# Kernel tuning notes

Measured on AMD Instinct MI355X. Metric: run time of the kernel, lower is better.

Reference implementation:

```python
import jax, jax.numpy as jnp
import numpy as np

# Gemma-2B style config
B, S, HID = 2, 2048, 2048
H, KH, D = 8, 1, 256          # query heads, kv heads, head_dim
THETA = 10000.0


def setup_inputs() -> dict:
    key = jax.random.key(0)
    ks = jax.random.split(key, 6)
    s = 0.02  # init scale for weights
    return {
        "hidden_states": jax.random.normal(ks[0], (B, S, HID), dtype=jnp.float32),
        "attention_mask": jnp.zeros((B, S), dtype=jnp.float32),  # additive mask over kv axis
        "position_ids": jnp.broadcast_to(jnp.arange(S, dtype=jnp.int32), (B, S)),
        "Wq": jax.random.normal(ks[1], (H * D, HID), dtype=jnp.float32) * s,
        "bq": jnp.zeros((H * D,), dtype=jnp.float32),
        "Wk": jax.random.normal(ks[2], (KH * D, HID), dtype=jnp.float32) * s,
        "bk": jnp.zeros((KH * D,), dtype=jnp.float32),
        "Wv": jax.random.normal(ks[3], (KH * D, HID), dtype=jnp.float32) * s,
        "bv": jnp.zeros((KH * D,), dtype=jnp.float32),
        "Wo": jax.random.normal(ks[4], (HID, H * D), dtype=jnp.float32) * s,
        "bo": jnp.zeros((HID,), dtype=jnp.float32),
    }


def _rope(x, position_ids):
    # x: [b, s, h, d]; rotate-half RoPE per head, computed in fp32 as in the module.
    half = D // 2
    inv_freq = 1.0 / (THETA ** (jnp.arange(0, D, 2, dtype=jnp.float32) / D))  # [d/2]
    freqs = position_ids.astype(jnp.float32)[:, :, None] * inv_freq            # [b, s, d/2]
    cos = jnp.cos(freqs)[:, :, None, :]  # [b, s, 1, d/2]
    sin = jnp.sin(freqs)[:, :, None, :]
    x1, x2 = x[..., :half], x[..., half:]
    return jnp.concatenate([cos * x1 - sin * x2, sin * x1 + cos * x2], axis=-1).astype(x.dtype)


def reference(hidden_states, attention_mask, position_ids, Wq, bq, Wk, bk, Wv, bv, Wo, bo):
    b, s, _ = hidden_states.shape
    q = (hidden_states @ Wq.T + bq).reshape(b, s, H, D)
    k = (hidden_states @ Wk.T + bk).reshape(b, s, KH, D)
    v = (hidden_states @ Wv.T + bv).reshape(b, s, KH, D)
    q = _rope(q, position_ids)
    k = _rope(k, position_ids)
    # GQA: broadcast the KV heads across query-head groups
    groups = H // KH
    k = jnp.repeat(k, groups, axis=2)  # [b, s, H, D]
    v = jnp.repeat(v, groups, axis=2)
    scores = jnp.einsum('bnhd,bmhd->bhnm', q, k) * (D ** -0.5)  # [b, H, s, s]
    scores = scores + attention_mask[:, None, None, :]
    attn = jax.nn.softmax(scores, axis=-1)  # dropout p=0.0 -> identity
    out = jnp.einsum('bhnm,bmhd->bnhd', attn, v).reshape(b, s, H * D)
    out = out @ Wo.T + bo
    return (out, attn)
```

## Files before the change

kernel.cpp:

```cpp
#include <hip/hip_runtime.h>

#define B_ 2
#define S_ 2048
#define HID_ 2048
#define H_ 8
#define D_ 256

typedef unsigned short u16;
typedef __attribute__((ext_vector_type(8))) short bf16x8;
typedef __attribute__((ext_vector_type(4))) float f32x4;

__device__ __forceinline__ u16 f2b(float x) {
    unsigned u = __float_as_uint(x);
    unsigned rb = (u >> 16) & 1u;
    u += 0x7fffu + rb;
    return (u16)(u >> 16);
}

__global__ __launch_bounds__(256) void cvt_bf16(const float* __restrict__ in,
                                                u16* __restrict__ out, int n) {
    int i = (blockIdx.x * 256 + threadIdx.x) * 4;
    if (i >= n) return;
    float4 f = *(const float4*)(in + i);
    union { u16 u[4]; uint2 v; } pk;
    pk.u[0] = f2b(f.x); pk.u[1] = f2b(f.y); pk.u[2] = f2b(f.z); pk.u[3] = f2b(f.w);
    *(uint2*)(out + i) = pk.v;
}

__global__ __launch_bounds__(256) void rope_kernel(const float* __restrict__ x,
                                                   const int* __restrict__ pos_ids,
                                                   u16* __restrict__ out, int nHeads) {
    int idx = blockIdx.x * 256 + threadIdx.x;
    int d   = idx & 127;
    int tmp = idx >> 7;
    int h   = tmp % nHeads;
    int n   = tmp / nHeads;
    int pos = pos_ids[n];
    float ang = (float)pos * expf(-(float)d * (9.210340371976184f / 128.0f));
    float s, c;
    sincosf(ang, &s, &c);
    size_t base = ((size_t)n * nHeads + h) * D_;
    float x1 = x[base + d], x2 = x[base + d + 128];
    out[base + d]       = f2b(c * x1 - s * x2);
    out[base + d + 128] = f2b(s * x1 + c * x2);
}

__global__ __launch_bounds__(256) void transpose_v(const float* __restrict__ v,
                                                   u16* __restrict__ vT) {
    __shared__ float t[32][33];
    int b = blockIdx.z;
    int s0 = blockIdx.x * 32, d0 = blockIdx.y * 32;
    int tx = threadIdx.x, ty = threadIdx.y;
#pragma unroll
    for (int i = 0; i < 4; ++i)
        t[ty + i * 8][tx] = v[(size_t)b * S_ * D_ + (size_t)(s0 + ty + i * 8) * D_ + d0 + tx];
    __syncthreads();
#pragma unroll
    for (int i = 0; i < 4; ++i)
        vT[(size_t)b * D_ * S_ + (size_t)(d0 + ty + i * 8) * S_ + s0 + tx] = f2b(t[tx][ty + i * 8]);
}

__global__ __launch_bounds__(256) void softmax_rows(float* __restrict__ attn,
                                                    const float* __restrict__ mask) {
    int row = blockIdx.x;
    int b = row >> 14;
    float* p = attn + (size_t)row * S_;
    const float* mb = mask + (size_t)b * S_;
    int t = threadIdx.x;
    const float sc = 0.0625f;

    float4 v0 = *(float4*)(p + t * 4);
    float4 v1 = *(float4*)(p + 1024 + t * 4);
    float4 m0 = *(const float4*)(mb + t * 4);
    float4 m1 = *(const float4*)(mb + 1024 + t * 4);
    float x[8] = { v0.x * sc + m0.x, v0.y * sc + m0.y, v0.z * sc + m0.z, v0.w * sc + m0.w,
                   v1.x * sc + m1.x, v1.y * sc + m1.y, v1.z * sc + m1.z, v1.w * sc + m1.w };

    float mx = x[0];
#pragma unroll
    for (int j = 1; j < 8; ++j) mx = fmaxf(mx, x[j]);
#pragma unroll
    for (int o = 32; o > 0; o >>= 1) mx = fmaxf(mx, __shfl_down(mx, o));
    __shared__ float redm[4], reds[4];
    int lane = t & 63, w = t >> 6;
    if (lane == 0) redm[w] = mx;
    __syncthreads();
    mx = fmaxf(fmaxf(redm[0], redm[1]), fmaxf(redm[2], redm[3]));

    float e[8], s = 0.f;
#pragma unroll
    for (int j = 0; j < 8; ++j) { e[j] = expf(x[j] - mx); s += e[j]; }
#pragma unroll
    for (int o = 32; o > 0; o >>= 1) s += __shfl_down(s, o);
    if (lane == 0) reds[w] = s;
    __syncthreads();
    s = reds[0] + reds[1] + reds[2] + reds[3];
    float inv = 1.f / s;

    float4 o0 = { e[0] * inv, e[1] * inv, e[2] * inv, e[3] * inv };
    float4 o1 = { e[4] * inv, e[5] * inv, e[6] * inv, e[7] * inv };
    *(float4*)(p + t * 4) = o0;
    *(float4*)(p + 1024 + t * 4) = o1;
}

#define TILE_M 128
#define TILE_N 128
#define TILE_K 32
#define LDSK 40

template <bool A_IS_F32, bool C_IS_BF16>
__global__ __launch_bounds__(256, 2) void gemm_bt(
    const void* __restrict__ Ap, const u16* __restrict__ Bp, void* __restrict__ Cp,
    const float* __restrict__ bias, int M, int N, int K, int lda, int ldb, int ldc,
    long sAb, long sAh, long sBb, long sBh, long sCb, long sCh, int numH) {
    __shared__ __align__(16) u16 As[TILE_M * LDSK];
    __shared__ __align__(16) u16 Bs[TILE_N * LDSK];

    int z = blockIdx.z;
    int bb = z / numH, hh = z % numH;
    const u16* A16 = nullptr;
    const float* Af = nullptr;
    if constexpr (A_IS_F32) Af = (const float*)Ap + (long)bb * sAb + (long)hh * sAh;
    else                    A16 = (const u16*)Ap + (long)bb * sAb + (long)hh * sAh;
    const u16* Bb = Bp + (long)bb * sBb + (long)hh * sBh;
    char* Cb = (char*)Cp;
    long cOff = (long)bb * sCb + (long)hh * sCh;

    const int m0 = blockIdx.y * TILE_M;
    const int n0 = blockIdx.x * TILE_N;
    const int tid = threadIdx.x;
    const int lane = tid & 63, wave = tid >> 6;
    const int l15 = lane & 15, quad = lane >> 4;
    const int waveM = wave >> 1, waveN = wave & 1;

    f32x4 acc[4][4];
#pragma unroll
    for (int mt = 0; mt < 4; ++mt)
#pragma unroll
        for (int nt = 0; nt < 4; ++nt)
#pragma unroll
            for (int r = 0; r < 4; ++r) acc[mt][nt][r] = 0.f;

    for (int k0 = 0; k0 < K; k0 += TILE_K) {
#pragma unroll
        for (int i = 0; i < 2; ++i) {
            int c = tid + i * 256;
            int row = c >> 2, col = (c & 3) * 8;
            if constexpr (A_IS_F32) {
                const float* src = Af + (size_t)(m0 + row) * lda + k0 + col;
                float4 f0 = *(const float4*)src;
                float4 f1 = *(const float4*)(src + 4);
                union { u16 u[8]; uint4 v; } pk;
                pk.u[0] = f2b(f0.x); pk.u[1] = f2b(f0.y); pk.u[2] = f2b(f0.z); pk.u[3] = f2b(f0.w);
                pk.u[4] = f2b(f1.x); pk.u[5] = f2b(f1.y); pk.u[6] = f2b(f1.z); pk.u[7] = f2b(f1.w);
                *(uint4*)&As[row * LDSK + col] = pk.v;
            } else {
                *(uint4*)&As[row * LDSK + col] =
                    *(const uint4*)(A16 + (size_t)(m0 + row) * lda + k0 + col);
            }
            *(uint4*)&Bs[row * LDSK + col] =
                *(const uint4*)(Bb + (size_t)(n0 + row) * ldb + k0 + col);
        }
        __syncthreads();

        bf16x8 av[4], bv[4];
#pragma unroll
        for (int t = 0; t < 4; ++t) {
            av[t] = *(bf16x8*)&As[(waveM * 64 + t * 16 + l15) * LDSK + quad * 8];
            bv[t] = *(bf16x8*)&Bs[(waveN * 64 + t * 16 + l15) * LDSK + quad * 8];
        }
#pragma unroll
        for (int mt = 0; mt < 4; ++mt)
#pragma unroll
            for (int nt = 0; nt < 4; ++nt)
                acc[mt][nt] = __builtin_amdgcn_mfma_f32_16x16x32_bf16(av[mt], bv[nt],
                                                                      acc[mt][nt], 0, 0, 0);
        __syncthreads();
    }

#pragma unroll
    for (int mt = 0; mt < 4; ++mt) {
        int row = m0 + waveM * 64 + mt * 16 + quad * 4;
#pragma unroll
        for (int nt = 0; nt < 4; ++nt) {
            int col = n0 + waveN * 64 + nt * 16 + l15;
            float bia = bias ? bias[col] : 0.f;
#pragma unroll
            for (int r = 0; r < 4; ++r) {
                float val = acc[mt][nt][r] + bia;
                if constexpr (C_IS_BF16)
                    ((u16*)Cb)[cOff + (size_t)(row + r) * ldc + col] = f2b(val);
                else
                    ((float*)Cb)[cOff + (size_t)(row + r) * ldc + col] = val;
            }
        }
    }
}

extern "C" void kernel_launch(void* const* d_in, const int* in_sizes, int n_in,
                              void* d_out, int out_size, void* d_ws, size_t ws_size,
                              hipStream_t stream) {
    const float* hs   = (const float*)d_in[0];
    const float* mask = (const float*)d_in[1];
    const int*   pos  = (const int*)d_in[2];
    const float* Wq = (const float*)d_in[3];
    const float* bq = (const float*)d_in[4];
    const float* Wk = (const float*)d_in[5];
    const float* bk = (const float*)d_in[6];
    const float* Wv = (const float*)d_in[7];
    const float* bv = (const float*)d_in[8];
    const float* Wo = (const float*)d_in[9];
    const float* bo = (const float*)d_in[10];

    float* out  = (float*)d_out;
    float* attn = (float*)d_out + (size_t)B_ * S_ * HID_;

    char* ws = (char*)d_ws;
    u16* hs_b   = (u16*)ws;                       ws += (size_t)B_ * S_ * HID_ * 2;
    u16* Wq_b   = (u16*)ws;                       ws += (size_t)H_ * D_ * HID_ * 2;
    u16* Wk_b   = (u16*)ws;                       ws += (size_t)D_ * HID_ * 2;
    u16* Wv_b   = (u16*)ws;                       ws += (size_t)D_ * HID_ * 2;
    u16* Wo_b   = (u16*)ws;                       ws += (size_t)HID_ * H_ * D_ * 2;
    float* q_f  = (float*)ws;                     ws += (size_t)B_ * S_ * H_ * D_ * 4;
    float* k_f  = (float*)ws;                     ws += (size_t)B_ * S_ * D_ * 4;
    float* v_f  = (float*)ws;                     ws += (size_t)B_ * S_ * D_ * 4;
    u16* q_b    = (u16*)ws;                       ws += (size_t)B_ * S_ * H_ * D_ * 2;
    u16* k_b    = (u16*)ws;                       ws += (size_t)B_ * S_ * D_ * 2;
    u16* vT_b   = (u16*)ws;                       ws += (size_t)B_ * D_ * S_ * 2;
    u16* ctx_b  = hs_b;

    cvt_bf16<<<dim3((B_ * S_ * HID_) / 1024), 256, 0, stream>>>(hs, hs_b, B_ * S_ * HID_);
    cvt_bf16<<<dim3((H_ * D_ * HID_) / 1024), 256, 0, stream>>>(Wq, Wq_b, H_ * D_ * HID_);
    cvt_bf16<<<dim3((D_ * HID_) / 1024), 256, 0, stream>>>(Wk, Wk_b, D_ * HID_);
    cvt_bf16<<<dim3((D_ * HID_) / 1024), 256, 0, stream>>>(Wv, Wv_b, D_ * HID_);
    cvt_bf16<<<dim3((HID_ * H_ * D_) / 1024), 256, 0, stream>>>(Wo, Wo_b, HID_ * H_ * D_);

    gemm_bt<false, false><<<dim3((H_ * D_) / TILE_N, (B_ * S_) / TILE_M, 1), 256, 0, stream>>>(
        hs_b, Wq_b, q_f, bq, B_ * S_, H_ * D_, HID_, HID_, HID_, H_ * D_,
        0, 0, 0, 0, 0, 0, 1);
    gemm_bt<false, false><<<dim3(D_ / TILE_N, (B_ * S_) / TILE_M, 1), 256, 0, stream>>>(
        hs_b, Wk_b, k_f, bk, B_ * S_, D_, HID_, HID_, HID_, D_,
        0, 0, 0, 0, 0, 0, 1);
    gemm_bt<false, false><<<dim3(D_ / TILE_N, (B_ * S_) / TILE_M, 1), 256, 0, stream>>>(
        hs_b, Wv_b, v_f, bv, B_ * S_, D_, HID_, HID_, HID_, D_,
        0, 0, 0, 0, 0, 0, 1);

    rope_kernel<<<dim3((B_ * S_ * H_ * 128) / 256), 256, 0, stream>>>(q_f, pos, q_b, H_);
    rope_kernel<<<dim3((B_ * S_ * 1 * 128) / 256), 256, 0, stream>>>(k_f, pos, k_b, 1);
    transpose_v<<<dim3(S_ / 32, D_ / 32, B_), dim3(32, 8), 0, stream>>>(v_f, vT_b);

    gemm_bt<false, false><<<dim3(S_ / TILE_N, S_ / TILE_M, B_ * H_), 256, 0, stream>>>(
        q_b, k_b, attn, nullptr, S_, S_, D_, H_ * D_, D_, S_,
        (long)S_ * H_ * D_, D_,
        (long)S_ * D_, 0,
        (long)H_ * S_ * S_, (long)S_ * S_,
        H_);

    softmax_rows<<<dim3(B_ * H_ * S_), 256, 0, stream>>>(attn, mask);

    gemm_bt<true, true><<<dim3(D_ / TILE_N, S_ / TILE_M, B_ * H_), 256, 0, stream>>>(
        attn, vT_b, ctx_b, nullptr, S_, D_, S_, S_, S_, H_ * D_,
        (long)H_ * S_ * S_, (long)S_ * S_,
        (long)D_ * S_, 0,
        (long)S_ * H_ * D_, D_,
        H_);

    gemm_bt<false, false><<<dim3(HID_ / TILE_N, (B_ * S_) / TILE_M, 1), 256, 0, stream>>>(
        ctx_b, Wo_b, out, bo, B_ * S_, HID_, H_ * D_, H_ * D_, H_ * D_, HID_,
        0, 0, 0, 0, 0, 0, 1);
}
```

Baseline: 818.8 us.

## Fuse QKV GEMM, use global_load_lds with swizzled LDS, emit bf16 attn

Concatenates the Q, K and V weights and biases into one GEMM launch and moves the GEMM tile loads to direct global-to-LDS async loads with an XOR-swizzled LDS layout instead of padded rows. When the workspace is large enough, softmax also writes a bf16 copy of the probabilities, so the PV GEMM reads bf16 directly rather than converting fp32 on the fly. This cuts register-staged copies, launches and PV read traffic, at the cost of an extra bf16 attention write and a workspace-size-dependent path.

```diff
diff --git a/kernel.cpp b/kernel.cpp
--- a/kernel.cpp
+++ b/kernel.cpp
@@ -5,6 +5,7 @@
 #define HID_ 2048
 #define H_ 8
 #define D_ 256
+#define NQKV 2560
 
 typedef unsigned short u16;
 typedef __attribute__((ext_vector_type(8))) short bf16x8;
@@ -15,6 +16,12 @@
     unsigned rb = (u >> 16) & 1u;
     u += 0x7fffu + rb;
     return (u16)(u >> 16);
+}
+
+__device__ __forceinline__ void load_lds16(const u16* g, u16* l) {
+    __builtin_amdgcn_global_load_lds(
+        (const __attribute__((address_space(1))) void*)g,
+        (__attribute__((address_space(3))) void*)l, 16, 0, 0);
 }
 
 __global__ __launch_bounds__(256) void cvt_bf16(const float* __restrict__ in,
@@ -27,7 +34,21 @@
     *(uint2*)(out + i) = pk.v;
 }
 
+__global__ __launch_bounds__(256) void concat_bias(const float* __restrict__ bq,
+                                                   const float* __restrict__ bk,
+                                                   const float* __restrict__ bv,
+                                                   float* __restrict__ dst) {
+    int i = blockIdx.x * 256 + threadIdx.x;
+    if (i >= NQKV) return;
+    float v;
+    if (i < H_ * D_) v = bq[i];
+    else if (i < H_ * D_ + D_) v = bk[i - H_ * D_];
+    else v = bv[i - H_ * D_ - D_];
+    dst[i] = v;
+}
+
 __global__ __launch_bounds__(256) void rope_kernel(const float* __restrict__ x,
+                                                   int rowStride, int colOff,
                                                    const int* __restrict__ pos_ids,
                                                    u16* __restrict__ out, int nHeads) {
     int idx = blockIdx.x * 256 + threadIdx.x;
@@ -39,13 +60,15 @@
     float ang = (float)pos * expf(-(float)d * (9.210340371976184f / 128.0f));
     float s, c;
     sincosf(ang, &s, &c);
-    size_t base = ((size_t)n * nHeads + h) * D_;
-    float x1 = x[base + d], x2 = x[base + d + 128];
-    out[base + d]       = f2b(c * x1 - s * x2);
-    out[base + d + 128] = f2b(s * x1 + c * x2);
+    size_t src = (size_t)n * rowStride + colOff + (size_t)h * D_;
+    float x1 = x[src + d], x2 = x[src + d + 128];
+    size_t dst = ((size_t)n * nHeads + h) * D_;
+    out[dst + d]       = f2b(c * x1 - s * x2);
+    out[dst + d + 128] = f2b(s * x1 + c * x2);
 }
 
 __global__ __launch_bounds__(256) void transpose_v(const float* __restrict__ v,
+                                                   int rowStride, int colOff,
                                                    u16* __restrict__ vT) {
     __shared__ float t[32][33];
     int b = blockIdx.z;
@@ -53,7 +76,7 @@
     int tx = threadIdx.x, ty = threadIdx.y;
 #pragma unroll
     for (int i = 0; i < 4; ++i)
-        t[ty + i * 8][tx] = v[(size_t)b * S_ * D_ + (size_t)(s0 + ty + i * 8) * D_ + d0 + tx];
+        t[ty + i * 8][tx] = v[((size_t)b * S_ + s0 + ty + i * 8) * rowStride + colOff + d0 + tx];
     __syncthreads();
 #pragma unroll
     for (int i = 0; i < 4; ++i)
@@ -61,7 +84,8 @@
 }
 
 __global__ __launch_bounds__(256) void softmax_rows(float* __restrict__ attn,
-                                                    const float* __restrict__ mask) {
+                                                    const float* __restrict__ mask,
+                                                    u16* __restrict__ attn_b) {
     int row = blockIdx.x;
     int b = row >> 14;
     float* p = attn + (size_t)row * S_;
@@ -97,33 +121,38 @@
     s = reds[0] + reds[1] + reds[2] + reds[3];
     float inv = 1.f / s;
 
-    float4 o0 = { e[0] * inv, e[1] * inv, e[2] * inv, e[3] * inv };
-    float4 o1 = { e[4] * inv, e[5] * inv, e[6] * inv, e[7] * inv };
-    *(float4*)(p + t * 4) = o0;
-    *(float4*)(p + 1024 + t * 4) = o1;
+    float o8[8];
+#pragma unroll
+    for (int j = 0; j < 8; ++j) o8[j] = e[j] * inv;
+    *(float4*)(p + t * 4)        = make_float4(o8[0], o8[1], o8[2], o8[3]);
+    *(float4*)(p + 1024 + t * 4) = make_float4(o8[4], o8[5], o8[6], o8[7]);
+
+    if (attn_b) {
+        u16* pb = attn_b + (size_t)row * S_;
+        union { u16 u[4]; uint2 v; } k0, k1;
+#pragma unroll
+        for (int j = 0; j < 4; ++j) { k0.u[j] = f2b(o8[j]); k1.u[j] = f2b(o8[4 + j]); }
+        *(uint2*)(pb + t * 4)        = k0.v;
+        *(uint2*)(pb + 1024 + t * 4) = k1.v;
+    }
 }
 
 #define TILE_M 128
 #define TILE_N 128
 #define TILE_K 32
-#define LDSK 40
-
-template <bool A_IS_F32, bool C_IS_BF16>
-__global__ __launch_bounds__(256, 2) void gemm_bt(
-    const void* __restrict__ Ap, const u16* __restrict__ Bp, void* __restrict__ Cp,
-    const float* __restrict__ bias, int M, int N, int K, int lda, int ldb, int ldc,
+
+template <bool C_IS_BF16>
+__global__ __launch_bounds__(256, 2) void gemm_async(
+    const u16* __restrict__ Ap, const u16* __restrict__ Bp, void* __restrict__ Cp,
+    const float* __restrict__ bias, int lda, int ldb, int ldc, int K,
     long sAb, long sAh, long sBb, long sBh, long sCb, long sCh, int numH) {
-    __shared__ __align__(16) u16 As[TILE_M * LDSK];
-    __shared__ __align__(16) u16 Bs[TILE_N * LDSK];
+    __shared__ __align__(16) u16 As[TILE_M * TILE_K];
+    __shared__ __align__(16) u16 Bs[TILE_N * TILE_K];
 
     int z = blockIdx.z;
     int bb = z / numH, hh = z % numH;
-    const u16* A16 = nullptr;
-    const float* Af = nullptr;
-    if constexpr (A_IS_F32) Af = (const float*)Ap + (long)bb * sAb + (long)hh * sAh;
-    else                    A16 = (const u16*)Ap + (long)bb * sAb + (long)hh * sAh;
+    const u16* Ab = Ap + (long)bb * sAb + (long)hh * sAh;
     const u16* Bb = Bp + (long)bb * sBb + (long)hh * sBh;
-    char* Cb = (char*)Cp;
     long cOff = (long)bb * sCb + (long)hh * sCh;
 
     const int m0 = blockIdx.y * TILE_M;
@@ -141,33 +170,32 @@
 #pragma unroll
             for (int r = 0; r < 4; ++r) acc[mt][nt][r] = 0.f;
 
+    int rowS[2], colS[2];
+    u16 *lA[2], *lB[2];
+#pragma unroll
+    for (int i = 0; i < 2; ++i) {
+        int c = i * 256 + tid;
+        rowS[i] = c >> 2;
+        colS[i] = (((c & 3) ^ ((rowS[i] >> 1) & 3)) * 8);
+        lA[i] = As + (size_t)(i * 256 + wave * 64) * 8;
+        lB[i] = Bs + (size_t)(i * 256 + wave * 64) * 8;
+    }
+
     for (int k0 = 0; k0 < K; k0 += TILE_K) {
 #pragma unroll
         for (int i = 0; i < 2; ++i) {
-            int c = tid + i * 256;
-            int row = c >> 2, col = (c & 3) * 8;
-            if constexpr (A_IS_F32) {
-                const float* src = Af + (size_t)(m0 + row) * lda + k0 + col;
-                float4 f0 = *(const float4*)src;
-                float4 f1 = *(const float4*)(src + 4);
-                union { u16 u[8]; uint4 v; } pk;
-                pk.u[0] = f2b(f0.x); pk.u[1] = f2b(f0.y); pk.u[2] = f2b(f0.z); pk.u[3] = f2b(f0.w);
-                pk.u[4] = f2b(f1.x); pk.u[5] = f2b(f1.y); pk.u[6] = f2b(f1.z); pk.u[7] = f2b(f1.w);
-                *(uint4*)&As[row * LDSK + col] = pk.v;
-            } else {
-                *(uint4*)&As[row * LDSK + col] =
-                    *(const uint4*)(A16 + (size_t)(m0 + row) * lda + k0 + col);
-            }
-            *(uint4*)&Bs[row * LDSK + col] =
-                *(const uint4*)(Bb + (size_t)(n0 + row) * ldb + k0 + col);
+            load_lds16(Ab + (size_t)(m0 + rowS[i]) * lda + k0 + colS[i], lA[i]);
+            load_lds16(Bb + (size_t)(n0 + rowS[i]) * ldb + k0 + colS[i], lB[i]);
         }
         __syncthreads();
 
         bf16x8 av[4], bv[4];
 #pragma unroll
         for (int t = 0; t < 4; ++t) {
-            av[t] = *(bf16x8*)&As[(waveM * 64 + t * 16 + l15) * LDSK + quad * 8];
-            bv[t] = *(bf16x8*)&Bs[(waveN * 64 + t * 16 + l15) * LDSK + quad * 8];
+            int ra = waveM * 64 + t * 16 + l15;
+            av[t] = *(bf16x8*)&As[ra * TILE_K + ((quad ^ ((ra >> 1) & 3)) * 8)];
+            int rb = waveN * 64 + t * 16 + l15;
+            bv[t] = *(bf16x8*)&Bs[rb * TILE_K + ((quad ^ ((rb >> 1) & 3)) * 8)];
         }
 #pragma unroll
         for (int mt = 0; mt < 4; ++mt)
@@ -189,10 +217,77 @@
             for (int r = 0; r < 4; ++r) {
                 float val = acc[mt][nt][r] + bia;
                 if constexpr (C_IS_BF16)
-                    ((u16*)Cb)[cOff + (size_t)(row + r) * ldc + col] = f2b(val);
+                    ((u16*)Cp)[cOff + (size_t)(row + r) * ldc + col] = f2b(val);
                 else
-                    ((float*)Cb)[cOff + (size_t)(row + r) * ldc + col] = val;
+                    ((float*)Cp)[cOff + (size_t)(row + r) * ldc + col] = val;
             }
+        }
+    }
+}
+
+#define LDSK 40
+__global__ __launch_bounds__(256, 2) void gemm_slow_f32a(
+    const float* __restrict__ Ap, const u16* __restrict__ Bp, u16* __restrict__ Cp,
+    int lda, int ldb, int ldc, int K,
+    long sAb, long sAh, long sBb, long sBh, long sCb, long sCh, int numH) {
+    __shared__ __align__(16) u16 As[TILE_M * LDSK];
+    __shared__ __align__(16) u16 Bs[TILE_N * LDSK];
+    int z = blockIdx.z;
+    int bb = z / numH, hh = z % numH;
+    const float* Af = Ap + (long)bb * sAb + (long)hh * sAh;
+    const u16* Bb = Bp + (long)bb * sBb + (long)hh * sBh;
+    long cOff = (long)bb * sCb + (long)hh * sCh;
+    const int m0 = blockIdx.y * TILE_M, n0 = blockIdx.x * TILE_N;
+    const int tid = threadIdx.x;
+    const int lane = tid & 63, wave = tid >> 6;
+    const int l15 = lane & 15, quad = lane >> 4;
+    const int waveM = wave >> 1, waveN = wave & 1;
+    f32x4 acc[4][4];
+#pragma unroll
+    for (int mt = 0; mt < 4; ++mt)
+#pragma unroll
+        for (int nt = 0; nt < 4; ++nt)
+#pragma unroll
+            for (int r = 0; r < 4; ++r) acc[mt][nt][r] = 0.f;
+    for (int k0 = 0; k0 < K; k0 += TILE_K) {
+#pragma unroll
+        for (int i = 0; i < 2; ++i) {
+            int c = tid + i * 256;
+            int row = c >> 2, col = (c & 3) * 8;
+            const float* src = Af + (size_t)(m0 + row) * lda + k0 + col;
+            float4 f0 = *(const float4*)src;
+            float4 f1 = *(const float4*)(src + 4);
+            union { u16 u[8]; uint4 v; } pk;
+            pk.u[0] = f2b(f0.x); pk.u[1] = f2b(f0.y); pk.u[2] = f2b(f0.z); pk.u[3] = f2b(f0.w);
+            pk.u[4] = f2b(f1.x); pk.u[5] = f2b(f1.y); pk.u[6] = f2b(f1.z); pk.u[7] = f2b(f1.w);
+            *(uint4*)&As[row * LDSK + col] = pk.v;
+            *(uint4*)&Bs[row * LDSK + col] =
+                *(const uint4*)(Bb + (size_t)(n0 + row) * ldb + k0 + col);
+        }
+        __syncthreads();
+        bf16x8 av[4], bv[4];
+#pragma unroll
+        for (int t = 0; t < 4; ++t) {
+            av[t] = *(bf16x8*)&As[(waveM * 64 + t * 16 + l15) * LDSK + quad * 8];
+            bv[t] = *(bf16x8*)&Bs[(waveN * 64 + t * 16 + l15) * LDSK + quad * 8];
+        }
+#pragma unroll
+        for (int mt = 0; mt < 4; ++mt)
+#pragma unroll
+            for (int nt = 0; nt < 4; ++nt)
+                acc[mt][nt] = __builtin_amdgcn_mfma_f32_16x16x32_bf16(av[mt], bv[nt],
+                                                                      acc[mt][nt], 0, 0, 0);
+        __syncthreads();
+    }
+#pragma unroll
+    for (int mt = 0; mt < 4; ++mt) {
+        int row = m0 + waveM * 64 + mt * 16 + quad * 4;
+#pragma unroll
+        for (int nt = 0; nt < 4; ++nt) {
+            int col = n0 + waveN * 64 + nt * 16 + l15;
+#pragma unroll
+            for (int r = 0; r < 4; ++r)
+                Cp[cOff + (size_t)(row + r) * ldc + col] = f2b(acc[mt][nt][r]);
         }
     }
 }
@@ -216,56 +311,65 @@
     float* attn = (float*)d_out + (size_t)B_ * S_ * HID_;
 
     char* ws = (char*)d_ws;
-    u16* hs_b   = (u16*)ws;                       ws += (size_t)B_ * S_ * HID_ * 2;
-    u16* Wq_b   = (u16*)ws;                       ws += (size_t)H_ * D_ * HID_ * 2;
-    u16* Wk_b   = (u16*)ws;                       ws += (size_t)D_ * HID_ * 2;
-    u16* Wv_b   = (u16*)ws;                       ws += (size_t)D_ * HID_ * 2;
-    u16* Wo_b   = (u16*)ws;                       ws += (size_t)HID_ * H_ * D_ * 2;
-    float* q_f  = (float*)ws;                     ws += (size_t)B_ * S_ * H_ * D_ * 4;
-    float* k_f  = (float*)ws;                     ws += (size_t)B_ * S_ * D_ * 4;
-    float* v_f  = (float*)ws;                     ws += (size_t)B_ * S_ * D_ * 4;
-    u16* q_b    = (u16*)ws;                       ws += (size_t)B_ * S_ * H_ * D_ * 2;
-    u16* k_b    = (u16*)ws;                       ws += (size_t)B_ * S_ * D_ * 2;
-    u16* vT_b   = (u16*)ws;                       ws += (size_t)B_ * D_ * S_ * 2;
-    u16* ctx_b  = hs_b;
+    size_t need = 0;
+    u16* hs_b    = (u16*)(ws);          need += (size_t)B_ * S_ * HID_ * 2;
+    u16* Wqkv_b  = (u16*)(ws + need);   need += (size_t)NQKV * HID_ * 2;
+    u16* Wo_b    = (u16*)(ws + need);   need += (size_t)HID_ * H_ * D_ * 2;
+    float* qkv_f = (float*)(ws + need); need += (size_t)B_ * S_ * NQKV * 4;
+    u16* q_b     = (u16*)(ws + need);   need += (size_t)B_ * S_ * H_ * D_ * 2;
+    u16* k_b     = (u16*)(ws + need);   need += (size_t)B_ * S_ * D_ * 2;
+    u16* vT_b    = (u16*)(ws + need);   need += (size_t)B_ * D_ * S_ * 2;
+    float* bqkv  = (float*)(ws + need); need += (size_t)NQKV * 4 + 4096;
+    need &= ~(size_t)255;
+    u16* attn_b  = (u16*)(ws + need);
+    size_t need_big = need + (size_t)B_ * H_ * S_ * S_ * 2;
+    bool big = ws_size >= need_big;
+    u16* ctx_b = hs_b;
 
     cvt_bf16<<<dim3((B_ * S_ * HID_) / 1024), 256, 0, stream>>>(hs, hs_b, B_ * S_ * HID_);
-    cvt_bf16<<<dim3((H_ * D_ * HID_) / 1024), 256, 0, stream>>>(Wq, Wq_b, H_ * D_ * HID_);
-    cvt_bf16<<<dim3((D_ * HID_) / 1024), 256, 0, stream>>>(Wk, Wk_b, D_ * HID_);
-    cvt_bf16<<<dim3((D_ * HID_) / 1024), 256, 0, stream>>>(Wv, Wv_b, D_ * HID_);
+    cvt_bf16<<<dim3((H_ * D_ * HID_) / 1024), 256, 0, stream>>>(Wq, Wqkv_b, H_ * D_ * HID_);
+    cvt_bf16<<<dim3((D_ * HID_) / 1024), 256, 0, stream>>>(Wk, Wqkv_b + (size_t)H_ * D_ * HID_, D_ * HID_);
+    cvt_bf16<<<dim3((D_ * HID_) / 1024), 256, 0, stream>>>(Wv, Wqkv_b + (size_t)(H_ * D_ + D_) * HID_, D_ * HID_);
     cvt_bf16<<<dim3((HID_ * H_ * D_) / 1024), 256, 0, stream>>>(Wo, Wo_b, HID_ * H_ * D_);
-
-    gemm_bt<false, false><<<dim3((H_ * D_) / TILE_N, (B_ * S_) / TILE_M, 1), 256, 0, stream>>>(
-        hs_b, Wq_b, q_f, bq, B_ * S_, H_ * D_, HID_, HID_, HID_, H_ * D_,
+    concat_bias<<<dim3((NQKV + 255) / 256), 256, 0, stream>>>(bq, bk, bv, bqkv);
+
+    gemm_async<false><<<dim3(NQKV / TILE_N, (B_ * S_) / TILE_M, 1), 256, 0, stream>>>(
+        hs_b, Wqkv_b, qkv_f, bqkv, HID_, HID_, NQKV, HID_,
         0, 0, 0, 0, 0, 0, 1);
-    gemm_bt<false, false><<<dim3(D_ / TILE_N, (B_ * S_) / TILE_M, 1), 256, 0, stream>>>(
-        hs_b, Wk_b, k_f, bk, B_ * S_, D_, HID_, HID_, HID_, D_,
-        0, 0, 0, 0, 0, 0, 1);
-    gemm_bt<false, false><<<dim3(D_ / TILE_N, (B_ * S_) / TILE_M, 1), 256, 0, stream>>>(
-        hs_b, Wv_b, v_f, bv, B_ * S_, D_, HID_, HID_, HID_, D_,
-        0, 0, 0, 0, 0, 0, 1);
-
-    rope_kernel<<<dim3((B_ * S_ * H_ * 128) / 256), 256, 0, stream>>>(q_f, pos, q_b, H_);
-    rope_kernel<<<dim3((B_ * S_ * 1 * 128) / 256), 256, 0, stream>>>(k_f, pos, k_b, 1);
-    transpose_v<<<dim3(S_ / 32, D_ / 32, B_), dim3(32, 8), 0, stream>>>(v_f, vT_b);
-
-    gemm_bt<false, false><<<dim3(S_ / TILE_N, S_ / TILE_M, B_ * H_), 256, 0, stream>>>(
-        q_b, k_b, attn, nullptr, S_, S_, D_, H_ * D_, D_, S_,
+
+    rope_kernel<<<dim3((B_ * S_ * H_ * 128) / 256), 256, 0, stream>>>(
+        qkv_f, NQKV, 0, pos, q_b, H_);
+    rope_kernel<<<dim3((B_ * S_ * 1 * 128) / 256), 256, 0, stream>>>(
+        qkv_f, NQKV, H_ * D_, pos, k_b, 1);
+    transpose_v<<<dim3(S_ / 32, D_ / 32, B_), dim3(32, 8), 0, stream>>>(
+        qkv_f, NQKV, H_ * D_ + D_, vT_b);
+
+    gemm_async<false><<<dim3(S_ / TILE_N, S_ / TILE_M, B_ * H_), 256, 0, stream>>>(
+        q_b, k_b, attn, nullptr, H_ * D_, D_, S_, D_,
         (long)S_ * H_ * D_, D_,
         (long)S_ * D_, 0,
         (long)H_ * S_ * S_, (long)S_ * S_,
         H_);
 
-    softmax_rows<<<dim3(B_ * H_ * S_), 256, 0, stream>>>(attn, mask);
-
-    gemm_bt<true, true><<<dim3(D_ / TILE_N, S_ / TILE_M, B_ * H_), 256, 0, stream>>>(
-        attn, vT_b, ctx_b, nullptr, S_, D_, S_, S_, S_, H_ * D_,
-        (long)H_ * S_ * S_, (long)S_ * S_,
-        (long)D_ * S_, 0,
-        (long)S_ * H_ * D_, D_,
-        H_);
-
-    gemm_bt<false, false><<<dim3(HID_ / TILE_N, (B_ * S_) / TILE_M, 1), 256, 0, stream>>>(
-        ctx_b, Wo_b, out, bo, B_ * S_, HID_, H_ * D_, H_ * D_, H_ * D_, HID_,
+    softmax_rows<<<dim3(B_ * H_ * S_), 256, 0, stream>>>(attn, mask, big ? attn_b : nullptr);
+
+    if (big) {
+        gemm_async<true><<<dim3(D_ / TILE_N, S_ / TILE_M, B_ * H_), 256, 0, stream>>>(
+            attn_b, vT_b, ctx_b, nullptr, S_, S_, H_ * D_, S_,
+            (long)H_ * S_ * S_, (long)S_ * S_,
+            (long)D_ * S_, 0,
+            (long)S_ * H_ * D_, D_,
+            H_);
+    } else {
+        gemm_slow_f32a<<<dim3(D_ / TILE_N, S_ / TILE_M, B_ * H_), 256, 0, stream>>>(
+            attn, vT_b, ctx_b, S_, S_, H_ * D_, S_,
+            (long)H_ * S_ * S_, (long)S_ * S_,
+            (long)D_ * S_, 0,
+            (long)S_ * H_ * D_, D_,
+            H_);
+    }
+
+    gemm_async<false><<<dim3(HID_ / TILE_N, (B_ * S_) / TILE_M, 1), 256, 0, stream>>>(
+        ctx_b, Wo_b, out, bo, H_ * D_, H_ * D_, HID_, H_ * D_,
         0, 0, 0, 0, 0, 0, 1);
 }
```

Measured after the change: 751.8 us. 1.09x faster.
